# Optimization experiments

Hardware: AMD Instinct MI355X
Metric: run time of the kernel (lower is better)

## Reference

```python
import jax, jax.numpy as jnp
import numpy as np

EPS = 1e-5
NEG_SLOPE = 0.2  # torch LeakyReLU default in DGCNN-style SharedMLPs


def knn_idx(p, k):
    # p: [B, 3, N]; returns idx [B, N, k] of k nearest neighbors (incl. self)
    inner = jnp.einsum('bdn,bdm->bnm', p, p)           # [B,N,N]
    sq = jnp.sum(p * p, axis=1)                         # [B,N]
    neg_dist = 2.0 * inner - sq[:, :, None] - sq[:, None, :]
    return jax.lax.top_k(neg_dist, k)[1]                # [B,N,k]


def smlp1d(x, w, b, g, bt):
    # x: [B,C,N]; 1x1 conv + BatchNorm1d (batch stats) + LeakyReLU
    y = jnp.einsum('bcn,oc->bon', x, w) + b[None, :, None]
    m = y.mean(axis=(0, 2), keepdims=True)
    v = y.var(axis=(0, 2), keepdims=True)
    y = g[None, :, None] * (y - m) * jax.lax.rsqrt(v + EPS) + bt[None, :, None]
    return jax.nn.leaky_relu(y, NEG_SLOPE)


def edgeconv(x, idx, w, b, g, bt):
    # x: [B,C,N], idx: [B,N,k] -> [B,O,N]
    B = x.shape[0]
    xT = jnp.transpose(x, (0, 2, 1))                    # [B,N,C]
    nb = xT[jnp.arange(B)[:, None, None], idx]          # [B,N,k,C] gather
    ctr = jnp.broadcast_to(xT[:, :, None, :], nb.shape)
    feat = jnp.concatenate([nb - ctr, ctr], axis=-1)    # [B,N,k,2C]
    y = jnp.einsum('bnkc,oc->bnko', feat, w) + b        # 1x1 conv2d
    m = y.mean(axis=(0, 1, 2), keepdims=True)
    v = y.var(axis=(0, 1, 2), keepdims=True)
    y = g * (y - m) * jax.lax.rsqrt(v + EPS) + bt
    y = jax.nn.leaky_relu(y, NEG_SLOPE)
    y = jnp.max(y, axis=2)                              # max over k -> [B,N,O]
    return jnp.transpose(y, (0, 2, 1))                  # [B,O,N]


def setup_inputs() -> dict:
    key = jax.random.key(0)
    ks = jax.random.split(key, 16)
    B, N, K = 2, 8192, 20
    C_in = 1024 + 3 * 64  # emb_dims + n_edgeconvs_backbone*64 = 1216
    OUT = 50

    def lin(k, o, c):
        return jax.random.normal(k, (o, c), jnp.float32) * (1.0 / np.sqrt(c))

    return {
        'x': jax.random.normal(ks[0], (B, C_in, N), jnp.float32),
        'p': jax.random.normal(ks[1], (B, 3, N), jnp.float32),
        # smlp1: 1216 -> 256
        'w1': lin(ks[2], 256, C_in), 'b1': jnp.zeros((256,), jnp.float32),
        'g1': jnp.ones((256,), jnp.float32), 'bt1': jnp.zeros((256,), jnp.float32),
        # edgeconv: 512 -> 256
        'we': lin(ks[3], 256, 512), 'be': jnp.zeros((256,), jnp.float32),
        'ge': jnp.ones((256,), jnp.float32), 'bte': jnp.zeros((256,), jnp.float32),
        # smlp2 part 1: 256 -> 256
        'w2': lin(ks[4], 256, 256), 'b2': jnp.zeros((256,), jnp.float32),
        'g2': jnp.ones((256,), jnp.float32), 'bt2': jnp.zeros((256,), jnp.float32),
        # smlp2 part 2: 256 -> 128
        'w3': lin(ks[5], 128, 256), 'b3': jnp.zeros((128,), jnp.float32),
        'g3': jnp.ones((128,), jnp.float32), 'bt3': jnp.zeros((128,), jnp.float32),
        # final conv1d: 128 -> 50
        'wf': lin(ks[6], OUT, 128), 'bf': jnp.zeros((OUT,), jnp.float32),
    }


def reference(x, p, w1, b1, g1, bt1, we, be, ge, bte,
              w2, b2, g2, bt2, w3, b3, g3, bt3, wf, bf):
    K = 20
    h = smlp1d(x, w1, b1, g1, bt1)              # [B,256,N]
    idx = knn_idx(p, K)                          # [B,N,K]
    h = edgeconv(h, idx, we, be, ge, bte)        # [B,256,N]
    h = smlp1d(h, w2, b2, g2, bt2)               # Dropout2d: identity (eval)
    h = smlp1d(h, w3, b3, g3, bt3)               # [B,128,N]
    return jnp.einsum('bcn,oc->bon', h, wf) + bf[None, :, None]  # [B,50,N]
```

## Files before the change

### kernel.cpp

```cpp
#include <hip/hip_runtime.h>

typedef unsigned short u16;
typedef unsigned int   u32;
typedef unsigned long long u64;
typedef __attribute__((ext_vector_type(4))) float f4;
typedef __attribute__((ext_vector_type(8))) short s8;
typedef __attribute__((ext_vector_type(4))) int   i4v;
typedef __attribute__((ext_vector_type(4))) unsigned short u16x4;

#define DEV __device__ __forceinline__

DEV u16 f2b(float f) {
  union { __bf16 b; u16 u; } c; c.b = (__bf16)f; return c.u;
}
DEV float b2f(u16 h) { return __uint_as_float(((u32)h) << 16); }

#define OFF_STATS 0L
#define OFF_W1B   65536L
#define OFF_WEAB  688128L
#define OFF_W2B   950272L
#define OFF_W3B   1081344L
#define OFF_IDX   1146880L
#define OFF_PQ    2457600L
#define OFF_Y1    44040192L
#define OFF_Y2    4194304L
#define OFF_EMAX  23068672L
#define OFF_EMIN  41943040L
#define OFF_Y3    4194304L
#define OFF_Y4    23068672L
#define WS_NEED   71303168L

__global__ __launch_bounds__(256) void k_convw(
    const float* __restrict__ w1, const float* __restrict__ we,
    const float* __restrict__ w2, const float* __restrict__ w3,
    const float* __restrict__ p,
    u16* __restrict__ w1b, u16* __restrict__ weABb,
    u16* __restrict__ w2b, u16* __restrict__ w3b, f4* __restrict__ pqg)
{
  int i = blockIdx.x * 256 + threadIdx.x;
  if (i < 311296) { w1b[i] = f2b(w1[i]); return; }
  i -= 311296;
  if (i < 131072) {
    int o = i >> 8, c = i & 255;
    float v = (o < 256) ? we[o * 512 + c]
                        : we[(o - 256) * 512 + 256 + c] - we[(o - 256) * 512 + c];
    weABb[i] = f2b(v); return;
  }
  i -= 131072;
  if (i < 65536) { w2b[i] = f2b(w2[i]); return; }
  i -= 65536;
  if (i < 32768) { w3b[i] = f2b(w3[i]); return; }
  i -= 32768;
  if (i < 16384) {
    int b = i >> 13, n = i & 8191;
    const float* pb = p + (long)b * 24576;
    float X = pb[n], Y = pb[8192 + n], Z = pb[16384 + n];
    f4 v; v[0] = X; v[1] = Y; v[2] = Z; v[3] = fmaf(X, X, fmaf(Y, Y, Z * Z));
    pqg[i] = v;
  }
}

__global__ __launch_bounds__(256) void k_knn(const f4* __restrict__ pqg, int* __restrict__ idxOut)
{
  __shared__ f4 chunk[1024];
  __shared__ u16 cand[4][4][128];
  __shared__ double ckeyv[4][128];
  __shared__ int scnt[4][4];
  const int tid = threadIdx.x, lane = tid & 63, w = tid >> 6;
  const int blk = blockIdx.x;
  const int b = blk >> 9;
  const int qbase = ((blk & 511) << 4) + (w << 2);
  const f4* __restrict__ P = pqg + ((long)b << 13);
  if (lane < 4) scnt[w][lane] = 0;
  float qx2[4], qy2[4], qz2[4];
#pragma unroll
  for (int j = 0; j < 4; ++j) {
    f4 Q = P[qbase + j];
    qx2[j] = Q[0] + Q[0]; qy2[j] = Q[1] + Q[1]; qz2[j] = Q[2] + Q[2];
  }
  float mx[4];
#pragma unroll
  for (int j = 0; j < 4; ++j) mx[j] = -3.0e38f;
  for (int c = 0; c < 8; ++c) {
    __syncthreads();
#pragma unroll
    for (int i = 0; i < 4; ++i) chunk[tid + i * 256] = P[c * 1024 + tid + i * 256];
    __syncthreads();
#pragma unroll 2
    for (int t = 0; t < 16; ++t) {
      f4 cc = chunk[(t << 6) + lane];
#pragma unroll
      for (int j = 0; j < 4; ++j) {
        float v = fmaf(qx2[j], cc[0], fmaf(qy2[j], cc[1], fmaf(qz2[j], cc[2], -cc[3])));
        mx[j] = fmaxf(mx[j], v);
      }
    }
  }
  float sv[4];
#pragma unroll
  for (int j = 0; j < 4; ++j) sv[j] = mx[j];
#pragma unroll
  for (int k = 2; k <= 64; k <<= 1) {
#pragma unroll
    for (int s = k >> 1; s > 0; s >>= 1) {
      const bool takeMin = (((lane & k) == 0) == ((lane & s) == 0));
#pragma unroll
      for (int j = 0; j < 4; ++j) {
        float o = __shfl_xor(sv[j], s);
        sv[j] = takeMin ? fminf(sv[j], o) : fmaxf(sv[j], o);
      }
    }
  }
  float T[4];
#pragma unroll
  for (int j = 0; j < 4; ++j) T[j] = __shfl(sv[j], 44) - 1e-3f;
  for (int c = 0; c < 8; ++c) {
    __syncthreads();
#pragma unroll
    for (int i = 0; i < 4; ++i) chunk[tid + i * 256] = P[c * 1024 + tid + i * 256];
    __syncthreads();
#pragma unroll 2
    for (int t = 0; t < 16; ++t) {
      f4 cc = chunk[(t << 6) + lane];
#pragma unroll
      for (int j = 0; j < 4; ++j) {
        float v = fmaf(qx2[j], cc[0], fmaf(qy2[j], cc[1], fmaf(qz2[j], cc[2], -cc[3])));
        if (v >= T[j]) {
          int pos = atomicAdd(&scnt[w][j], 1);
          if (pos < 128) cand[w][j][pos] = (u16)(c * 1024 + (t << 6) + lane);
        }
      }
    }
  }
  asm volatile("s_waitcnt lgkmcnt(0)" ::: "memory");
  for (int j = 0; j < 4; ++j) {
    int cn = scnt[w][j]; if (cn > 128) cn = 128;
    f4 Q = P[qbase + j];
    const double Qx = (double)Q[0], Qy = (double)Q[1], Qz = (double)Q[2];
    const double Qs = Qx * Qx + Qy * Qy + Qz * Qz;
    double myV[2]; int myI[2];
#pragma unroll
    for (int jj = 0; jj < 2; ++jj) {
      const int e = lane + (jj << 6);
      myV[jj] = -1.0e300; myI[jj] = 0x7FFFFFFF;
      if (e < cn) {
        const int ci = cand[w][j][e];
        f4 c = P[ci];
        double cx = (double)c[0], cy = (double)c[1], cz = (double)c[2];
        double v = 2.0 * (Qx * cx + Qy * cy + Qz * cz) - Qs - (cx * cx + cy * cy + cz * cz);
        myV[jj] = v; myI[jj] = ci;
        ckeyv[w][e] = v;
      }
    }
    asm volatile("s_waitcnt lgkmcnt(0)" ::: "memory");
    int rk0 = 0, rk1 = 0;
#pragma unroll 4
    for (int e2 = 0; e2 < cn; ++e2) {
      double ov = ckeyv[w][e2];
      int oi = (int)cand[w][j][e2];
      rk0 += ((ov > myV[0]) || (ov == myV[0] && oi < myI[0])) ? 1 : 0;
      rk1 += ((ov > myV[1]) || (ov == myV[1] && oi < myI[1])) ? 1 : 0;
    }
    int* orow = idxOut + (((long)b << 13) + qbase + j) * 20;
    if (lane < cn && rk0 < 20) orow[rk0] = myI[0];
    if (lane + 64 < cn && rk1 < 20) orow[rk1] = myI[1];
    asm volatile("s_waitcnt lgkmcnt(0)" ::: "memory");
  }
}

DEV float lky(float z) { return z > 0.f ? z : 0.2f * z; }

DEV i4v applyPack8(i4v raw, const float* sc, const float* sh, int kb) {
  u16 r[8];
#pragma unroll
  for (int e = 0; e < 8; ++e) {
    u32 dw = (u32)raw[e >> 1];
    u16 h = (e & 1) ? (u16)(dw >> 16) : (u16)(dw & 0xFFFFu);
    r[e] = f2b(lky(fmaf(sc[kb + e], b2f(h), sh[kb + e])));
  }
  i4v o;
#pragma unroll
  for (int e = 0; e < 4; ++e) o[e] = (int)((u32)r[2 * e] | ((u32)r[2 * e + 1] << 16));
  return o;
}

DEV i4v selPack8b(i4v rawM, i4v rawN, const float* sc, const float* sh, int kb) {
  u16 r[8];
#pragma unroll
  for (int e = 0; e < 8; ++e) {
    u32 dM = (u32)rawM[e >> 1], dN = (u32)rawN[e >> 1];
    u16 hM = (e & 1) ? (u16)(dM >> 16) : (u16)(dM & 0xFFFFu);
    u16 hN = (e & 1) ? (u16)(dN >> 16) : (u16)(dN & 0xFFFFu);
    float s = sc[kb + e];
    float y = (s >= 0.f) ? b2f(hM) : b2f(hN);
    r[e] = f2b(lky(fmaf(s, y, sh[kb + e])));
  }
  i4v o;
#pragma unroll
  for (int e = 0; e < 4; ++e) o[e] = (int)((u32)r[2 * e] | ((u32)r[2 * e + 1] << 16));
  return o;
}

#define XSTRIDE 130
DEV s8 packFrag(const float* __restrict__ sBf, int kb, int nl) {
  union { u16 u[8]; s8 v; } r;
#pragma unroll
  for (int i = 0; i < 8; ++i) r.u[i] = f2b(sBf[(kb + i) * XSTRIDE + nl]);
  return r.v;
}

template<int BMODE, int STATS, int BF16OUT>
__global__ __launch_bounds__(256, 2) void k_gemm(
    const u16* __restrict__ A, const void* __restrict__ B0v, const void* __restrict__ B1v,
    const float* __restrict__ sums, const float* __restrict__ ssq,
    const float* __restrict__ g, const float* __restrict__ bt, float invCount,
    float* __restrict__ gsums, float* __restrict__ gssq,
    void* __restrict__ Yv, int M, int K, long strideB, long strideY)
{
  __shared__ u16 sA[2][4096];
  __shared__ __align__(16) char sBr[2][(BMODE == 3) ? 16640 : 8192];
  __shared__ float scB[256], shB[256];
  __shared__ float s_sum[128], s_ssq[128];
  const int b = blockIdx.z;
  const int m0 = blockIdx.y * 128;
  const int n0 = blockIdx.x * 128;
  const int tid = threadIdx.x, lane = tid & 63, w = tid >> 6;
  const int wr = w >> 1, wc = w & 1;
  const int r15 = lane & 15, g8 = (lane >> 4) * 8;

  if (BMODE == 1 || BMODE == 2) {
    float m = sums[tid] * invCount;
    float v = ssq[tid] * invCount - m * m;
    float s = g[tid] / sqrtf(v + 1e-5f);
    scB[tid] = s;
    shB[tid] = bt[tid] - m * s;
  }
  if (STATS) { if (tid < 128) { s_sum[tid] = 0.f; s_ssq[tid] = 0.f; } }
  if (BMODE == 1 || BMODE == 2) __syncthreads();

  f4 acc[4][4];
#pragma unroll
  for (int i = 0; i < 4; ++i)
#pragma unroll
    for (int j = 0; j < 4; ++j) { f4 z = {0.f, 0.f, 0.f, 0.f}; acc[i][j] = z; }

  const int row0 = tid >> 2;
  const int kp0 = (tid & 3) << 3;
  const u16* gA0 = A + (long)(m0 + row0) * K + kp0;
  const u16* gA1 = A + (long)(m0 + row0 + 64) * K + kp0;
  const int ch0 = tid, ch1 = tid + 256;

  const u16* gB0 = (const u16*)B0v + (long)b * strideB + (long)(n0 + row0) * K + kp0;
  const u16* gB1 = gB0 + (long)64 * K;
  const u16* nB0 = (const u16*)B1v + (long)b * strideB + (long)(n0 + row0) * K + kp0;
  const u16* nB1 = nB0 + (long)64 * K;
  const float* xB = (const float*)B0v + (long)b * strideB;
  const int kS = tid >> 3, nS = (tid & 7) << 2;
  const float* gX = xB + (long)kS * 8192 + n0 + nS;

  ((i4v*)sA[0])[ch0] = *(const i4v*)gA0;
  ((i4v*)sA[0])[ch1] = *(const i4v*)gA1;
  if (BMODE == 0) {
    ((i4v*)sBr[0])[ch0] = *(const i4v*)gB0;
    ((i4v*)sBr[0])[ch1] = *(const i4v*)gB1;
  } else if (BMODE == 1) {
    ((i4v*)sBr[0])[ch0] = applyPack8(*(const i4v*)gB0, scB, shB, kp0);
    ((i4v*)sBr[0])[ch1] = applyPack8(*(const i4v*)gB1, scB, shB, kp0);
  } else if (BMODE == 2) {
    ((i4v*)sBr[0])[ch0] = selPack8b(*(const i4v*)gB0, *(const i4v*)nB0, scB, shB, kp0);
    ((i4v*)sBr[0])[ch1] = selPack8b(*(const i4v*)gB1, *(const i4v*)nB1, scB, shB, kp0);
  } else {
    float* sBf0 = (float*)sBr[0];
#pragma unroll
    for (int it = 0; it < 4; ++it) {
      f4 v = *(const f4*)(gX + it * 32);
      float* dst = sBf0 + kS * XSTRIDE + nS + it * 32;
      ((float2*)dst)[0] = make_float2(v[0], v[1]);
      ((float2*)dst)[1] = make_float2(v[2], v[3]);
    }
  }
  __syncthreads();

  const int KT = K >> 5;
  int cur = 0;
  for (int kk = 0; kk < KT; ++kk) {
    const bool more = (kk + 1 < KT);
    i4v ra0, ra1, rb0, rb1, rn0, rn1;
    f4 xv[4];
    if (more) {
      long ko = (long)(kk + 1) * 32;
      ra0 = *(const i4v*)(gA0 + ko); ra1 = *(const i4v*)(gA1 + ko);
      if (BMODE == 0 || BMODE == 1) {
        rb0 = *(const i4v*)(gB0 + ko); rb1 = *(const i4v*)(gB1 + ko);
      } else if (BMODE == 2) {
        rb0 = *(const i4v*)(gB0 + ko); rb1 = *(const i4v*)(gB1 + ko);
        rn0 = *(const i4v*)(nB0 + ko); rn1 = *(const i4v*)(nB1 + ko);
      } else {
        const float* gx = gX + ko * 8192;
#pragma unroll
        for (int it = 0; it < 4; ++it) xv[it] = *(const f4*)(gx + it * 32);
      }
    }
    const u16* la = sA[cur];
    s8 af[4], bfr[4];
#pragma unroll
    for (int mi = 0; mi < 4; ++mi)
      af[mi] = *(const s8*)(la + (wr * 64 + mi * 16 + r15) * 32 + g8);
    if (BMODE == 3) {
      const float* sBfc = (const float*)sBr[cur];
#pragma unroll
      for (int ni = 0; ni < 4; ++ni)
        bfr[ni] = packFrag(sBfc, g8, wc * 64 + ni * 16 + r15);
    } else {
      const u16* lb = (const u16*)sBr[cur];
#pragma unroll
      for (int ni = 0; ni < 4; ++ni)
        bfr[ni] = *(const s8*)(lb + (wc * 64 + ni * 16 + r15) * 32 + g8);
    }
#pragma unroll
    for (int mi = 0; mi < 4; ++mi)
#pragma unroll
      for (int ni = 0; ni < 4; ++ni)
        acc[mi][ni] = __builtin_amdgcn_mfma_f32_16x16x32_bf16(af[mi], bfr[ni], acc[mi][ni], 0, 0, 0);
    if (more) {
      ((i4v*)sA[cur ^ 1])[ch0] = ra0; ((i4v*)sA[cur ^ 1])[ch1] = ra1;
      if (BMODE == 0) {
        ((i4v*)sBr[cur ^ 1])[ch0] = rb0; ((i4v*)sBr[cur ^ 1])[ch1] = rb1;
      } else if (BMODE == 1) {
        const int kb = (kk + 1) * 32 + kp0;
        ((i4v*)sBr[cur ^ 1])[ch0] = applyPack8(rb0, scB, shB, kb);
        ((i4v*)sBr[cur ^ 1])[ch1] = applyPack8(rb1, scB, shB, kb);
      } else if (BMODE == 2) {
        const int kb = (kk + 1) * 32 + kp0;
        ((i4v*)sBr[cur ^ 1])[ch0] = selPack8b(rb0, rn0, scB, shB, kb);
        ((i4v*)sBr[cur ^ 1])[ch1] = selPack8b(rb1, rn1, scB, shB, kb);
      } else {
        float* sBfn = (float*)sBr[cur ^ 1];
#pragma unroll
        for (int it = 0; it < 4; ++it) {
          float* dst = sBfn + kS * XSTRIDE + nS + it * 32;
          ((float2*)dst)[0] = make_float2(xv[it][0], xv[it][1]);
          ((float2*)dst)[1] = make_float2(xv[it][2], xv[it][3]);
        }
      }
    }
    __syncthreads();
    cur ^= 1;
  }
  const int og = m0 + wr * 64 + (lane >> 4) * 4;
  const int ng = n0 + wc * 64 + r15;
  if (BF16OUT) {
    u16* Yp = (u16*)Yv + (long)b * strideY;
#pragma unroll
    for (int mi = 0; mi < 4; ++mi)
#pragma unroll
      for (int ni = 0; ni < 4; ++ni) {
        f4 a = acc[mi][ni];
        u16x4 r;
#pragma unroll
        for (int q = 0; q < 4; ++q) r[q] = f2b(a[q]);
        *(u16x4*)(Yp + (long)(ng + ni * 16) * M + og + mi * 16) = r;
      }
  } else {
    float* Yp = (float*)Yv + (long)b * strideY;
#pragma unroll
    for (int mi = 0; mi < 4; ++mi)
#pragma unroll
      for (int ni = 0; ni < 4; ++ni)
        *(f4*)(Yp + (long)(ng + ni * 16) * M + og + mi * 16) = acc[mi][ni];
  }
  if (STATS) {
#pragma unroll
    for (int mi = 0; mi < 4; ++mi)
#pragma unroll
      for (int j = 0; j < 4; ++j) {
        float s = 0.f, q = 0.f;
#pragma unroll
        for (int ni = 0; ni < 4; ++ni) {
          float v = acc[mi][ni][j];
          s += v; q = fmaf(v, v, q);
        }
#pragma unroll
        for (int off = 1; off < 16; off <<= 1) {
          s += __shfl_xor(s, off);
          q += __shfl_xor(q, off);
        }
        if ((lane & 15) == 0) {
          int lc = wr * 64 + (lane >> 4) * 4 + mi * 16 + j;
          atomicAdd(&s_sum[lc], s);
          atomicAdd(&s_ssq[lc], q);
        }
      }
    __syncthreads();
    if (tid < 128) {
      atomicAdd(&gsums[m0 + tid], s_sum[tid]);
      atomicAdd(&gssq[m0 + tid], s_ssq[tid]);
    }
  }
}

__global__ __launch_bounds__(256, 2) void k_edge_gather(
    const u16* __restrict__ Y2, const int* __restrict__ idx,
    u16* __restrict__ Emax, u16* __restrict__ Emin,
    float* __restrict__ sums, float* __restrict__ ssq)
{
  __shared__ float s_sum[256], s_ssq[256];
  const int tid = threadIdx.x, lane = tid & 63, w = tid >> 6;
  s_sum[tid] = 0.f; s_ssq[tid] = 0.f;
  __syncthreads();
  const int half = blockIdx.y, b = blockIdx.z;
  const int ptBase = blockIdx.x * 64 + w * 16;
  const int sub = lane >> 5;
  const int chOff = half * 128 + ((lane & 31) << 2);
  f4 lsum = {0.f, 0.f, 0.f, 0.f}, lssq = {0.f, 0.f, 0.f, 0.f};
  for (int i = 0; i < 8; ++i) {
    const int pt = ptBase + i * 2 + sub;
    const long gp = (long)b * 8192 + pt;
    u16x4 cr = *(const u16x4*)(Y2 + gp * 512 + 256 + chOff);
    f4 ctr; ctr[0] = b2f(cr[0]); ctr[1] = b2f(cr[1]); ctr[2] = b2f(cr[2]); ctr[3] = b2f(cr[3]);
    const int* irow = idx + gp * 20;
    f4 vmax = {-3.0e38f, -3.0e38f, -3.0e38f, -3.0e38f};
    f4 vmin = {3.0e38f, 3.0e38f, 3.0e38f, 3.0e38f};
#pragma unroll 4
    for (int k = 0; k < 20; ++k) {
      int m = irow[k];
      u16x4 nr = *(const u16x4*)(Y2 + ((long)b * 8192 + m) * 512 + chOff);
#pragma unroll
      for (int j = 0; j < 4; ++j) {
        float y = b2f(nr[j]) + ctr[j];
        vmax[j] = fmaxf(vmax[j], y);
        vmin[j] = fminf(vmin[j], y);
        lsum[j] += y;
        lssq[j] = fmaf(y, y, lssq[j]);
      }
    }
    u16x4 eM, eN;
#pragma unroll
    for (int j = 0; j < 4; ++j) { eM[j] = f2b(vmax[j]); eN[j] = f2b(vmin[j]); }
    *(u16x4*)(Emax + gp * 256 + chOff) = eM;
    *(u16x4*)(Emin + gp * 256 + chOff) = eN;
  }
#pragma unroll
  for (int j = 0; j < 4; ++j) {
    atomicAdd(&s_sum[chOff + j], lsum[j]);
    atomicAdd(&s_ssq[chOff + j], lssq[j]);
  }
  __syncthreads();
  atomicAdd(&sums[tid], s_sum[tid]);
  atomicAdd(&ssq[tid], s_ssq[tid]);
}

__global__ __launch_bounds__(64) void k_final(
    const float* __restrict__ Y4, const float* __restrict__ sums, const float* __restrict__ ssq,
    const float* __restrict__ g, const float* __restrict__ bt,
    const float* __restrict__ wf, const float* __restrict__ bf,
    float* __restrict__ out)
{
  __shared__ float swf[128][56];
  __shared__ float sc[128], sh[128], sb[52];
  const int lane = threadIdx.x;
  if (lane < 50) {
    const float* wrow = wf + lane * 128;
#pragma unroll 8
    for (int ch = 0; ch < 128; ++ch) swf[ch][lane] = wrow[ch];
    sb[lane] = bf[lane];
  } else if (lane < 52) {
#pragma unroll 8
    for (int ch = 0; ch < 128; ++ch) swf[ch][lane] = 0.f;
    sb[lane] = 0.f;
  }
#pragma unroll
  for (int t = 0; t < 2; ++t) {
    int ch = lane + t * 64;
    float m = sums[ch] * (1.0f / 16384.0f);
    float v = ssq[ch] * (1.0f / 16384.0f) - m * m;
    float s = g[ch] / sqrtf(v + 1e-5f);
    sc[ch] = s;
    sh[ch] = bt[ch] - m * s;
  }
  __syncthreads();
  const int b = blockIdx.y;
  const int n = blockIdx.x * 64 + lane;
  const float* hp = Y4 + ((long)b * 8192 + n) * 128;
  f4 av[13];
#pragma unroll
  for (int i = 0; i < 13; ++i) { f4 z = {0.f, 0.f, 0.f, 0.f}; av[i] = z; }
#pragma unroll 4
  for (int c4 = 0; c4 < 32; ++c4) {
    f4 hv = *(const f4*)(hp + c4 * 4);
#pragma unroll
    for (int e = 0; e < 4; ++e) {
      const int ch = c4 * 4 + e;
      float z = lky(fmaf(sc[ch], hv[e], sh[ch]));
#pragma unroll
      for (int o4 = 0; o4 < 13; ++o4) {
        f4 wv = *(const f4*)&swf[ch][o4 * 4];
#pragma unroll
        for (int q = 0; q < 4; ++q) av[o4][q] = fmaf(z, wv[q], av[o4][q]);
      }
    }
  }
  float* ob = out + (((long)b * 50) << 13) + n;
#pragma unroll
  for (int o4 = 0; o4 < 13; ++o4)
#pragma unroll
    for (int q = 0; q < 4; ++q) {
      int o = o4 * 4 + q;
      if (o < 50) ob[(long)o << 13] = av[o4][q] + sb[o];
    }
}

extern "C" void kernel_launch(void* const* d_in, const int* in_sizes, int n_in,
                              void* d_out, int out_size, void* d_ws, size_t ws_size,
                              hipStream_t stream)
{
  if ((long)ws_size < WS_NEED) return;
  const float* x   = (const float*)d_in[0];
  const float* p   = (const float*)d_in[1];
  const float* w1  = (const float*)d_in[2];
  const float* g1w = (const float*)d_in[4];
  const float* bt1 = (const float*)d_in[5];
  const float* we  = (const float*)d_in[6];
  const float* gew = (const float*)d_in[8];
  const float* bte = (const float*)d_in[9];
  const float* w2  = (const float*)d_in[10];
  const float* g2w = (const float*)d_in[12];
  const float* bt2 = (const float*)d_in[13];
  const float* w3  = (const float*)d_in[14];
  const float* g3w = (const float*)d_in[16];
  const float* bt3 = (const float*)d_in[17];
  const float* wf  = (const float*)d_in[18];
  const float* bfi = (const float*)d_in[19];

  char* ws = (char*)d_ws;
  u16* w1b   = (u16*)(ws + OFF_W1B);
  u16* weABb = (u16*)(ws + OFF_WEAB);
  u16* w2b   = (u16*)(ws + OFF_W2B);
  u16* w3b   = (u16*)(ws + OFF_W3B);
  int* idxb  = (int*)(ws + OFF_IDX);
  f4*  pqg   = (f4*)(ws + OFF_PQ);
  u16*   Y1b  = (u16*)(ws + OFF_Y1);
  u16*   Y2b  = (u16*)(ws + OFF_Y2);
  u16*   EMAX = (u16*)(ws + OFF_EMAX);
  u16*   EMIN = (u16*)(ws + OFF_EMIN);
  u16*   Y3b  = (u16*)(ws + OFF_Y3);
  float* Y4   = (float*)(ws + OFF_Y4);
  float* st0 = (float*)(ws + OFF_STATS);
  float* st1 = (float*)(ws + OFF_STATS + 4096);
  float* st2 = (float*)(ws + OFF_STATS + 8192);
  float* st3 = (float*)(ws + OFF_STATS + 12288);

  hipMemsetAsync(ws + OFF_STATS, 0, 16384, stream);
  k_convw<<<2176, 256, 0, stream>>>(w1, we, w2, w3, p, w1b, weABb, w2b, w3b, pqg);
  k_knn<<<1024, 256, 0, stream>>>(pqg, idxb);

  k_gemm<3, 1, 1><<<dim3(64, 2, 2), 256, 0, stream>>>(
      w1b, x, nullptr, nullptr, nullptr, nullptr, nullptr, 0.f,
      st0, st0 + 256, Y1b, 256, 1216, (long)1216 * 8192, (long)8192 * 256);

  k_gemm<1, 0, 1><<<dim3(64, 4, 2), 256, 0, stream>>>(
      weABb, Y1b, nullptr, st0, st0 + 256, g1w, bt1, 1.0f / 16384.0f,
      nullptr, nullptr, Y2b, 512, 256, (long)8192 * 256, (long)8192 * 512);

  k_edge_gather<<<dim3(128, 2, 2), 256, 0, stream>>>(Y2b, idxb, EMAX, EMIN, st1, st1 + 256);

  k_gemm<2, 1, 1><<<dim3(64, 2, 2), 256, 0, stream>>>(
      w2b, EMAX, EMIN, st1, st1 + 256, gew, bte, 1.0f / 327680.0f,
      st2, st2 + 256, Y3b, 256, 256, (long)8192 * 256, (long)8192 * 256);

  k_gemm<1, 1, 0><<<dim3(64, 1, 2), 256, 0, stream>>>(
      w3b, Y3b, nullptr, st2, st2 + 256, g2w, bt2, 1.0f / 16384.0f,
      st3, st3 + 256, Y4, 128, 256, (long)8192 * 256, (long)8192 * 128);

  k_final<<<dim3(128, 2), 64, 0, stream>>>(Y4, st3, st3 + 256, g3w, bt3, wf, bfi, (float*)d_out);
}
```

Baseline: 216.1 us.

## Fuse kNN and first GEMM into one heterogeneous kernel launch

Merges the kNN kernel and the first 1216->256 GEMM into a single launch of 1280 blocks. Every fifth block runs a GEMM tile and the remaining blocks run kNN query groups, with both sharing one union shared-memory buffer. The two independent stages can then run concurrently on the GPU instead of back to back, so each fills idle CUs during the other. The cost is a larger shared-memory footprint for kNN blocks and different occupancy (launch bounds now 3), and the generic GEMM template drops its unused float-input path.

Measured after the change: 237.9 us. +10.1%, slower.

```diff
diff --git a/kernel.cpp b/kernel.cpp
--- a/kernel.cpp
+++ b/kernel.cpp
@@ -60,16 +60,157 @@
   }
 }
 
-__global__ __launch_bounds__(256) void k_knn(const f4* __restrict__ pqg, int* __restrict__ idxOut)
+DEV float lky(float z) { return z > 0.f ? z : 0.2f * z; }
+
+#define XSTRIDE 130
+DEV s8 packFragU(const float* __restrict__ sBf, int kb, int nl) {
+  union { u16 u[8]; s8 v; } r;
+#pragma unroll
+  for (int i = 0; i < 8; ++i) r.u[i] = f2b(sBf[(kb + i) * XSTRIDE + nl]);
+  return r.v;
+}
+
+__global__ __launch_bounds__(256, 3) void k_knn_g1(
+    const f4* __restrict__ pqg, int* __restrict__ idxOut,
+    const u16* __restrict__ A, const float* __restrict__ x,
+    float* __restrict__ gsums, float* __restrict__ gssq, u16* __restrict__ Y1b)
 {
-  __shared__ f4 chunk[1024];
-  __shared__ u16 cand[4][4][128];
-  __shared__ double ckeyv[4][128];
-  __shared__ int scnt[4][4];
+  __shared__ __align__(16) char U[50688];
+  const int blk = blockIdx.x;
   const int tid = threadIdx.x, lane = tid & 63, w = tid >> 6;
-  const int blk = blockIdx.x;
-  const int b = blk >> 9;
-  const int qbase = ((blk & 511) << 4) + (w << 2);
+
+  if ((blk % 5) == 4) {
+    const int gid = blk / 5;
+    const int b = gid >> 7;
+    const int m0 = ((gid >> 6) & 1) * 128;
+    const int n0 = (gid & 63) * 128;
+    const int K = 1216, M = 256;
+    u16* sA = (u16*)U;
+    float* s_sum = (float*)(U + 49664);
+    float* s_ssq = (float*)(U + 50176);
+    const int wr = w >> 1, wc = w & 1;
+    const int r15 = lane & 15, g8 = (lane >> 4) * 8;
+    if (tid < 128) { s_sum[tid] = 0.f; s_ssq[tid] = 0.f; }
+
+    f4 acc[4][4];
+#pragma unroll
+    for (int i = 0; i < 4; ++i)
+#pragma unroll
+      for (int j = 0; j < 4; ++j) { f4 z = {0.f, 0.f, 0.f, 0.f}; acc[i][j] = z; }
+
+    const int row0 = tid >> 2;
+    const int kp0 = (tid & 3) << 3;
+    const u16* gA0 = A + (long)(m0 + row0) * K + kp0;
+    const u16* gA1 = A + (long)(m0 + row0 + 64) * K + kp0;
+    const int ch0 = tid, ch1 = tid + 256;
+    const int kS = tid >> 3, nS = (tid & 7) << 2;
+    const float* gX = x + (long)b * 1216 * 8192 + (long)kS * 8192 + n0 + nS;
+
+    ((i4v*)sA)[ch0] = *(const i4v*)gA0;
+    ((i4v*)sA)[ch1] = *(const i4v*)gA1;
+    {
+      float* sBf0 = (float*)(U + 16384);
+#pragma unroll
+      for (int it = 0; it < 4; ++it) {
+        f4 v = *(const f4*)(gX + it * 32);
+        float* dst = sBf0 + kS * XSTRIDE + nS + it * 32;
+        ((float2*)dst)[0] = make_float2(v[0], v[1]);
+        ((float2*)dst)[1] = make_float2(v[2], v[3]);
+      }
+    }
+    __syncthreads();
+
+    const int KT = K >> 5;
+    int cur = 0;
+    for (int kk = 0; kk < KT; ++kk) {
+      const bool more = (kk + 1 < KT);
+      i4v ra0, ra1;
+      f4 xv[4];
+      if (more) {
+        long ko = (long)(kk + 1) * 32;
+        ra0 = *(const i4v*)(gA0 + ko); ra1 = *(const i4v*)(gA1 + ko);
+        const float* gx = gX + ko * 8192;
+#pragma unroll
+        for (int it = 0; it < 4; ++it) xv[it] = *(const f4*)(gx + it * 32);
+      }
+      const u16* la = sA + cur * 4096;
+      const float* sBfc = (const float*)(U + 16384 + cur * 16640);
+      s8 af[4], bfr[4];
+#pragma unroll
+      for (int mi = 0; mi < 4; ++mi)
+        af[mi] = *(const s8*)(la + (wr * 64 + mi * 16 + r15) * 32 + g8);
+#pragma unroll
+      for (int ni = 0; ni < 4; ++ni)
+        bfr[ni] = packFragU(sBfc, g8, wc * 64 + ni * 16 + r15);
+#pragma unroll
+      for (int mi = 0; mi < 4; ++mi)
+#pragma unroll
+        for (int ni = 0; ni < 4; ++ni)
+          acc[mi][ni] = __builtin_amdgcn_mfma_f32_16x16x32_bf16(af[mi], bfr[ni], acc[mi][ni], 0, 0, 0);
+      if (more) {
+        u16* na = sA + (cur ^ 1) * 4096;
+        ((i4v*)na)[ch0] = ra0;
+        ((i4v*)na)[ch1] = ra1;
+        float* sBfn = (float*)(U + 16384 + (cur ^ 1) * 16640);
+#pragma unroll
+        for (int it = 0; it < 4; ++it) {
+          float* dst = sBfn + kS * XSTRIDE + nS + it * 32;
+          ((float2*)dst)[0] = make_float2(xv[it][0], xv[it][1]);
+          ((float2*)dst)[1] = make_float2(xv[it][2], xv[it][3]);
+        }
+      }
+      __syncthreads();
+      cur ^= 1;
+    }
+    const int og = m0 + wr * 64 + (lane >> 4) * 4;
+    const int ng = n0 + wc * 64 + r15;
+    u16* Yp = Y1b + (long)b * 8192 * 256;
+#pragma unroll
+    for (int mi = 0; mi < 4; ++mi)
+#pragma unroll
+      for (int ni = 0; ni < 4; ++ni) {
+        f4 a = acc[mi][ni];
+        u16x4 r;
+#pragma unroll
+        for (int q = 0; q < 4; ++q) r[q] = f2b(a[q]);
+        *(u16x4*)(Yp + (long)(ng + ni * 16) * M + og + mi * 16) = r;
+      }
+#pragma unroll
+    for (int mi = 0; mi < 4; ++mi)
+#pragma unroll
+      for (int j = 0; j < 4; ++j) {
+        float s = 0.f, q = 0.f;
+#pragma unroll
+        for (int ni = 0; ni < 4; ++ni) {
+          float v = acc[mi][ni][j];
+          s += v; q = fmaf(v, v, q);
+        }
+#pragma unroll
+        for (int off = 1; off < 16; off <<= 1) {
+          s += __shfl_xor(s, off);
+          q += __shfl_xor(q, off);
+        }
+        if ((lane & 15) == 0) {
+          int lc = wr * 64 + (lane >> 4) * 4 + mi * 16 + j;
+          atomicAdd(&s_sum[lc], s);
+          atomicAdd(&s_ssq[lc], q);
+        }
+      }
+    __syncthreads();
+    if (tid < 128) {
+      atomicAdd(&gsums[m0 + tid], s_sum[tid]);
+      atomicAdd(&gssq[m0 + tid], s_ssq[tid]);
+    }
+    return;
+  }
+
+  const int kid = (blk / 5) * 4 + (blk % 5);
+  f4* chunk = (f4*)U;
+  u16 (*cand)[4][128] = (u16(*)[4][128])(U + 16384);
+  double (*ckeyv)[128] = (double(*)[128])(U + 20480);
+  int (*scnt)[4] = (int(*)[4])(U + 24576);
+  const int b = kid >> 9;
+  const int qbase = ((kid & 511) << 4) + (w << 2);
   const f4* __restrict__ P = pqg + ((long)b << 13);
   if (lane < 4) scnt[w][lane] = 0;
   float qx2[4], qy2[4], qz2[4];
@@ -168,8 +309,6 @@
   }
 }
 
-DEV float lky(float z) { return z > 0.f ? z : 0.2f * z; }
-
 DEV i4v applyPack8(i4v raw, const float* sc, const float* sh, int kb) {
   u16 r[8];
 #pragma unroll
@@ -199,14 +338,6 @@
 #pragma unroll
   for (int e = 0; e < 4; ++e) o[e] = (int)((u32)r[2 * e] | ((u32)r[2 * e + 1] << 16));
   return o;
-}
-
-#define XSTRIDE 130
-DEV s8 packFrag(const float* __restrict__ sBf, int kb, int nl) {
-  union { u16 u[8]; s8 v; } r;
-#pragma unroll
-  for (int i = 0; i < 8; ++i) r.u[i] = f2b(sBf[(kb + i) * XSTRIDE + nl]);
-  return r.v;
 }
 
 template<int BMODE, int STATS, int BF16OUT>
@@ -218,7 +349,7 @@
     void* __restrict__ Yv, int M, int K, long strideB, long strideY)
 {
   __shared__ u16 sA[2][4096];
-  __shared__ __align__(16) char sBr[2][(BMODE == 3) ? 16640 : 8192];
+  __shared__ __align__(16) u16 sB[2][4096];
   __shared__ float scB[256], shB[256];
   __shared__ float s_sum[128], s_ssq[128];
   const int b = blockIdx.z;
@@ -228,7 +359,7 @@
   const int wr = w >> 1, wc = w & 1;
   const int r15 = lane & 15, g8 = (lane >> 4) * 8;
 
-  if (BMODE == 1 || BMODE == 2) {
+  {
     float m = sums[tid] * invCount;
     float v = ssq[tid] * invCount - m * m;
     float s = g[tid] / sqrtf(v + 1e-5f);
@@ -236,7 +367,7 @@
     shB[tid] = bt[tid] - m * s;
   }
   if (STATS) { if (tid < 128) { s_sum[tid] = 0.f; s_ssq[tid] = 0.f; } }
-  if (BMODE == 1 || BMODE == 2) __syncthreads();
+  __syncthreads();
 
   f4 acc[4][4];
 #pragma unroll
@@ -254,31 +385,16 @@
   const u16* gB1 = gB0 + (long)64 * K;
   const u16* nB0 = (const u16*)B1v + (long)b * strideB + (long)(n0 + row0) * K + kp0;
   const u16* nB1 = nB0 + (long)64 * K;
-  const float* xB = (const float*)B0v + (long)b * strideB;
-  const int kS = tid >> 3, nS = (tid & 7) << 2;
-  const float* gX = xB + (long)kS * 8192 + n0 + nS;
-
+
+  if (BMODE == 1) {
+    ((i4v*)sB[0])[ch0] = applyPack8(*(const i4v*)gB0, scB, shB, kp0);
+    ((i4v*)sB[0])[ch1] = applyPack8(*(const i4v*)gB1, scB, shB, kp0);
+  } else {
+    ((i4v*)sB[0])[ch0] = selPack8b(*(const i4v*)gB0, *(const i4v*)nB0, scB, shB, kp0);
+    ((i4v*)sB[0])[ch1] = selPack8b(*(const i4v*)gB1, *(const i4v*)nB1, scB, shB, kp0);
+  }
   ((i4v*)sA[0])[ch0] = *(const i4v*)gA0;
   ((i4v*)sA[0])[ch1] = *(const i4v*)gA1;
-  if (BMODE == 0) {
-    ((i4v*)sBr[0])[ch0] = *(const i4v*)gB0;
-    ((i4v*)sBr[0])[ch1] = *(const i4v*)gB1;
-  } else if (BMODE == 1) {
-    ((i4v*)sBr[0])[ch0] = applyPack8(*(const i4v*)gB0, scB, shB, kp0);
-    ((i4v*)sBr[0])[ch1] = applyPack8(*(const i4v*)gB1, scB, shB, kp0);
-  } else if (BMODE == 2) {
-    ((i4v*)sBr[0])[ch0] = selPack8b(*(const i4v*)gB0, *(const i4v*)nB0, scB, shB, kp0);
-    ((i4v*)sBr[0])[ch1] = selPack8b(*(const i4v*)gB1, *(const i4v*)nB1, scB, shB, kp0);
-  } else {
-    float* sBf0 = (float*)sBr[0];
-#pragma unroll
-    for (int it = 0; it < 4; ++it) {
-      f4 v = *(const f4*)(gX + it * 32);
-      float* dst = sBf0 + kS * XSTRIDE + nS + it * 32;
-      ((float2*)dst)[0] = make_float2(v[0], v[1]);
-      ((float2*)dst)[1] = make_float2(v[2], v[3]);
-    }
-  }
   __syncthreads();
 
   const int KT = K >> 5;
@@ -286,37 +402,21 @@
   for (int kk = 0; kk < KT; ++kk) {
     const bool more = (kk + 1 < KT);
     i4v ra0, ra1, rb0, rb1, rn0, rn1;
-    f4 xv[4];
     if (more) {
       long ko = (long)(kk + 1) * 32;
       ra0 = *(const i4v*)(gA0 + ko); ra1 = *(const i4v*)(gA1 + ko);
-      if (BMODE == 0 || BMODE == 1) {
-        rb0 = *(const i4v*)(gB0 + ko); rb1 = *(const i4v*)(gB1 + ko);
-      } else if (BMODE == 2) {
-        rb0 = *(const i4v*)(gB0 + ko); rb1 = *(const i4v*)(gB1 + ko);
-        rn0 = *(const i4v*)(nB0 + ko); rn1 = *(const i4v*)(nB1 + ko);
-      } else {
-        const float* gx = gX + ko * 8192;
-#pragma unroll
-        for (int it = 0; it < 4; ++it) xv[it] = *(const f4*)(gx + it * 32);
-      }
+      rb0 = *(const i4v*)(gB0 + ko); rb1 = *(const i4v*)(gB1 + ko);
+      if (BMODE == 2) { rn0 = *(const i4v*)(nB0 + ko); rn1 = *(const i4v*)(nB1 + ko); }
     }
     const u16* la = sA[cur];
+    const u16* lb = sB[cur];
     s8 af[4], bfr[4];
 #pragma unroll
     for (int mi = 0; mi < 4; ++mi)
       af[mi] = *(const s8*)(la + (wr * 64 + mi * 16 + r15) * 32 + g8);
-    if (BMODE == 3) {
-      const float* sBfc = (const float*)sBr[cur];
-#pragma unroll
-      for (int ni = 0; ni < 4; ++ni)
-        bfr[ni] = packFrag(sBfc, g8, wc * 64 + ni * 16 + r15);
-    } else {
-      const u16* lb = (const u16*)sBr[cur];
-#pragma unroll
-      for (int ni = 0; ni < 4; ++ni)
-        bfr[ni] = *(const s8*)(lb + (wc * 64 + ni * 16 + r15) * 32 + g8);
-    }
+#pragma unroll
+    for (int ni = 0; ni < 4; ++ni)
+      bfr[ni] = *(const s8*)(lb + (wc * 64 + ni * 16 + r15) * 32 + g8);
 #pragma unroll
     for (int mi = 0; mi < 4; ++mi)
 #pragma unroll
@@ -324,24 +424,13 @@
         acc[mi][ni] = __builtin_amdgcn_mfma_f32_16x16x32_bf16(af[mi], bfr[ni], acc[mi][ni], 0, 0, 0);
     if (more) {
       ((i4v*)sA[cur ^ 1])[ch0] = ra0; ((i4v*)sA[cur ^ 1])[ch1] = ra1;
-      if (BMODE == 0) {
-        ((i4v*)sBr[cur ^ 1])[ch0] = rb0; ((i4v*)sBr[cur ^ 1])[ch1] = rb1;
-      } else if (BMODE == 1) {
-        const int kb = (kk + 1) * 32 + kp0;
-        ((i4v*)sBr[cur ^ 1])[ch0] = applyPack8(rb0, scB, shB, kb);
-        ((i4v*)sBr[cur ^ 1])[ch1] = applyPack8(rb1, scB, shB, kb);
-      } else if (BMODE == 2) {
-        const int kb = (kk + 1) * 32 + kp0;
-        ((i4v*)sBr[cur ^ 1])[ch0] = selPack8b(rb0, rn0, scB, shB, kb);
-        ((i4v*)sBr[cur ^ 1])[ch1] = selPack8b(rb1, rn1, scB, shB, kb);
+      const int kb = (kk + 1) * 32 + kp0;
+      if (BMODE == 1) {
+        ((i4v*)sB[cur ^ 1])[ch0] = applyPack8(rb0, scB, shB, kb);
+        ((i4v*)sB[cur ^ 1])[ch1] = applyPack8(rb1, scB, shB, kb);
       } else {
-        float* sBfn = (float*)sBr[cur ^ 1];
-#pragma unroll
-        for (int it = 0; it < 4; ++it) {
-          float* dst = sBfn + kS * XSTRIDE + nS + it * 32;
-          ((float2*)dst)[0] = make_float2(xv[it][0], xv[it][1]);
-          ((float2*)dst)[1] = make_float2(xv[it][2], xv[it][3]);
-        }
+        ((i4v*)sB[cur ^ 1])[ch0] = selPack8b(rb0, rn0, scB, shB, kb);
+        ((i4v*)sB[cur ^ 1])[ch1] = selPack8b(rb1, rn1, scB, shB, kb);
       }
     }
     __syncthreads();
@@ -552,11 +641,8 @@
 
   hipMemsetAsync(ws + OFF_STATS, 0, 16384, stream);
   k_convw<<<2176, 256, 0, stream>>>(w1, we, w2, w3, p, w1b, weABb, w2b, w3b, pqg);
-  k_knn<<<1024, 256, 0, stream>>>(pqg, idxb);
-
-  k_gemm<3, 1, 1><<<dim3(64, 2, 2), 256, 0, stream>>>(
-      w1b, x, nullptr, nullptr, nullptr, nullptr, nullptr, 0.f,
-      st0, st0 + 256, Y1b, 256, 1216, (long)1216 * 8192, (long)8192 * 256);
+
+  k_knn_g1<<<1280, 256, 0, stream>>>(pqg, idxb, w1b, x, st0, st0 + 256, Y1b);
 
   k_gemm<1, 0, 1><<<dim3(64, 4, 2), 256, 0, stream>>>(
       weABb, Y1b, nullptr, st0, st0 + 256, g1w, bt1, 1.0f / 16384.0f,
```
